# Kernel optimization log

Measured on AMD Instinct MI355X. Metric: run time of the kernel, lower is better.

Reference implementation:

```python
import jax, jax.numpy as jnp
import numpy as np

NUM_EMBEDDINGS = 1024
EMBEDDING_DIM = 64
COMMITMENT_COST = 0.25


def setup_inputs() -> dict:
    key = jax.random.key(0)
    k_in, k_cb = jax.random.split(key)
    inputs = jax.random.normal(k_in, (32, 4096, EMBEDDING_DIM), dtype=jnp.float32)
    # matches reset_embeddings(): uniform(-1/num_embeddings, 1/num_embeddings)
    bound = 1.0 / NUM_EMBEDDINGS
    codebook = jax.random.uniform(k_cb, (NUM_EMBEDDINGS, EMBEDDING_DIM),
                                  dtype=jnp.float32, minval=-bound, maxval=bound)
    return {"inputs": inputs, "codebook": codebook}


def reference(inputs, codebook):
    input_shape = inputs.shape
    D = codebook.shape[1]
    x = inputs.reshape(-1, D)  # [N, D]
    # Squared euclidean distances; argmin is invariant to the sqrt used by torch.cdist.
    # dist2[n,k] = ||x_n||^2 - 2 x_n . e_k + ||e_k||^2
    dist2 = (jnp.sum(x * x, axis=1, keepdims=True)
             - 2.0 * (x @ codebook.T)
             + jnp.sum(codebook * codebook, axis=1))  # [N, K]
    encoding_indices = jnp.argmin(dist2, axis=1)  # [N]
    quantized = codebook[encoding_indices].reshape(input_shape)
    loss = (jnp.mean((jax.lax.stop_gradient(quantized) - inputs) ** 2)
            + COMMITMENT_COST * jnp.mean((quantized - jax.lax.stop_gradient(inputs)) ** 2))
    # straight-through estimator
    quantized_st = inputs + jax.lax.stop_gradient(quantized - inputs)
    return quantized_st, loss
```

## Files before the change

### kernel.cpp

```cpp
#include <hip/hip_runtime.h>


typedef __attribute__((ext_vector_type(8))) short short8;
typedef __attribute__((ext_vector_type(4))) float f32x4;

#define VQ_D 64
#define MTILE 512
#define NTH 512
#define CSTRIDE 68

__device__ inline unsigned short f2bf(float f) {
  union { float f; unsigned u; } v; v.f = f;
  unsigned r = v.u + 0x7FFFu + ((v.u >> 16) & 1u);
  return (unsigned short)(r >> 16);
}

__global__ __launch_bounds__(256) void vq_prep(const float* __restrict__ cb,
                                               float* __restrict__ c2b,
                                               unsigned short* __restrict__ cbb,
                                               float* __restrict__ sse,
                                               unsigned* __restrict__ counter, int K) {
  if (blockIdx.x == 0 && threadIdx.x == 0) { *sse = 0.f; *counter = 0u; }
  int w = (int)((blockIdx.x * 256 + threadIdx.x) >> 6);
  int lane = threadIdx.x & 63;
  if (w >= K) return;
  float v = cb[(size_t)w * VQ_D + lane];
  cbb[(size_t)w * CSTRIDE + lane] = f2bf(v);
  if (lane < CSTRIDE - VQ_D) cbb[(size_t)w * CSTRIDE + VQ_D + lane] = 0;
  float s = v * v;
#pragma unroll
  for (int off = 32; off; off >>= 1) s += __shfl_down(s, off);
  if (lane == 0) c2b[w] = s + 0.5f;
}

__global__ __launch_bounds__(NTH) void vq_main(
    const float* __restrict__ x, const float* __restrict__ cb,
    const float* __restrict__ c2b, const unsigned short* __restrict__ cbb,
    float* __restrict__ out, float* __restrict__ sse_out,
    unsigned* __restrict__ counter, int nblocks) {
  __shared__ unsigned short cbs[1024 * CSTRIDE];
  __shared__ float c2s[1024];
  __shared__ int idxs[MTILE];
  __shared__ float redbuf[8];

  const int tid = threadIdx.x;
  const int wave = tid >> 6;
  const int lane = tid & 63;
  const int quad = lane >> 4;
  const int col = lane & 15;
  const long blockRow0 = (long)blockIdx.x * MTILE;
  const int waveRow0 = wave * 64;

  const char* gbase = (const char*)cbb;
#pragma unroll
  for (int i = 0; i < 17; ++i) {
    const int chunk0 = i * NTH + wave * 64;
    const char* src = gbase + (size_t)(chunk0 + lane) * 16;
    __builtin_amdgcn_global_load_lds(
        (const __attribute__((address_space(1))) void*)src,
        (__attribute__((address_space(3))) void*)(cbs + (size_t)chunk0 * 8),
        16, 0, 0);
  }
  c2s[tid] = c2b[tid];
  c2s[tid + 512] = c2b[tid + 512];

  short8 Af[4][2];
#pragma unroll
  for (int mi = 0; mi < 4; ++mi) {
#pragma unroll
    for (int ks = 0; ks < 2; ++ks) {
      long row = blockRow0 + waveRow0 + mi * 16 + col;
      const f32x4* xp = (const f32x4*)(x + row * VQ_D + ks * 32 + quad * 8);
      f32x4 lo = xp[0];
      f32x4 hi = xp[1];
      short8 a;
      a[0] = (short)f2bf(-2.f * lo[0]); a[1] = (short)f2bf(-2.f * lo[1]);
      a[2] = (short)f2bf(-2.f * lo[2]); a[3] = (short)f2bf(-2.f * lo[3]);
      a[4] = (short)f2bf(-2.f * hi[0]); a[5] = (short)f2bf(-2.f * hi[1]);
      a[6] = (short)f2bf(-2.f * hi[2]); a[7] = (short)f2bf(-2.f * hi[3]);
      Af[mi][ks] = a;
    }
  }

  unsigned bk[4][4];
#pragma unroll
  for (int mi = 0; mi < 4; ++mi)
#pragma unroll
    for (int r = 0; r < 4; ++r) bk[mi][r] = 0xFFFFFFFFu;

  __syncthreads();

  const unsigned short* bbase = cbs + (size_t)col * CSTRIDE + quad * 8;
#pragma unroll 4
  for (int t = 0; t < 64; ++t) {
    const unsigned short* bp = bbase + t * 16 * CSTRIDE;
    short8 b0 = *(const short8*)bp;
    short8 b1 = *(const short8*)(bp + 32);
    float cc = c2s[t * 16 + col];

    f32x4 acc[4];
#pragma unroll
    for (int mi = 0; mi < 4; ++mi) {
      f32x4 a = {cc, cc, cc, cc};
      a = __builtin_amdgcn_mfma_f32_16x16x32_bf16(Af[mi][0], b0, a, 0, 0, 0);
      a = __builtin_amdgcn_mfma_f32_16x16x32_bf16(Af[mi][1], b1, a, 0, 0, 0);
      acc[mi] = a;
    }

    const unsigned code = (unsigned)((t << 4) + col);
#pragma unroll
    for (int mi = 0; mi < 4; ++mi)
#pragma unroll
      for (int r = 0; r < 4; ++r)
        bk[mi][r] = min(bk[mi][r], (__float_as_uint(acc[mi][r]) & 0xFFFFFC00u) | code);
  }

#pragma unroll
  for (int off = 1; off < 16; off <<= 1) {
#pragma unroll
    for (int mi = 0; mi < 4; ++mi)
#pragma unroll
      for (int r = 0; r < 4; ++r) {
        unsigned o = (unsigned)__shfl_xor((int)bk[mi][r], off);
        bk[mi][r] = min(bk[mi][r], o);
      }
  }
  if (col == 0) {
#pragma unroll
    for (int mi = 0; mi < 4; ++mi)
#pragma unroll
      for (int r = 0; r < 4; ++r)
        idxs[waveRow0 + mi * 16 + quad * 4 + r] = (int)(bk[mi][r] & 1023u);
  }
  __syncthreads();

  float sse = 0.f;
  const f32x4* x4 = (const f32x4*)x;
  f32x4* out4 = (f32x4*)out;
#pragma unroll
  for (int i = 0; i < 16; ++i) {
    int f = i * NTH + tid;
    int row_l = f >> 4;
    int d4 = f & 15;
    int idx = idxs[row_l];
    unsigned long long ev =
        *(const unsigned long long*)(cbs + (size_t)idx * CSTRIDE + d4 * 4);
    f32x4 cv;
    cv[0] = __uint_as_float((unsigned)(ev & 0xFFFFull) << 16);
    cv[1] = __uint_as_float((unsigned)((ev >> 16) & 0xFFFFull) << 16);
    cv[2] = __uint_as_float((unsigned)((ev >> 32) & 0xFFFFull) << 16);
    cv[3] = __uint_as_float((unsigned)((ev >> 48) & 0xFFFFull) << 16);
    long gi = (blockRow0 + row_l) * 16 + d4;
    f32x4 xv = x4[gi];
    out4[gi] = cv;
    f32x4 dv = cv - xv;
    sse += dv[0] * dv[0] + dv[1] * dv[1] + dv[2] * dv[2] + dv[3] * dv[3];
  }
#pragma unroll
  for (int off = 32; off; off >>= 1) sse += __shfl_down(sse, off);
  if (lane == 0) redbuf[wave] = sse;
  __syncthreads();

  if (tid == 0) {
    float s = 0.f;
#pragma unroll
    for (int w = 0; w < 8; ++w) s += redbuf[w];
    atomicAdd(sse_out, s);
    __threadfence();
    unsigned old = atomicAdd(counter, 1u);
    if (old == (unsigned)(nblocks - 1)) {
      float tot = atomicAdd(sse_out, 0.f);
      long nelem = (long)nblocks * MTILE * VQ_D;
      out[nelem] = 1.25f * tot / (float)nelem;
    }
  }
}

extern "C" void kernel_launch(void* const* d_in, const int* in_sizes, int n_in,
                              void* d_out, int out_size, void* d_ws, size_t ws_size,
                              hipStream_t stream) {
  const float* x = (const float*)d_in[0];
  const float* cb = (const float*)d_in[1];
  float* out = (float*)d_out;

  const long n_elem = (long)in_sizes[0];
  const int nrows = (int)(n_elem / VQ_D);
  const int K = in_sizes[1] / VQ_D;
  const int nblocks = nrows / MTILE;

  char* ws = (char*)d_ws;
  float* sse = (float*)ws;
  unsigned* counter = (unsigned*)(ws + 64);
  float* c2b = (float*)(ws + 256);
  unsigned short* cbb = (unsigned short*)(ws + 8192);

  vq_prep<<<dim3((K * 64 + 255) / 256), dim3(256), 0, stream>>>(cb, c2b, cbb, sse, counter, K);
  vq_main<<<dim3(nblocks), dim3(NTH), 0, stream>>>(x, cb, c2b, cbb, out, sse, counter, nblocks);
}
```

Measured before the change: 132.2 us.

## Derive SSE from argmin distance and split codebook gather into separate kernel

The loss is now computed algebraically from the minimum distance value kept in the packed argmin key plus the per-row input norm. This removes the second read of x and the per-element difference loop. The output gather moves to a separate kernel that copies fp32 codebook rows by index from a global index buffer. This also fixes the old path writing bf16-rounded codebook values. The risk is that the SSE is less exact: the distance key is bf16-based and its low 10 bits are truncated. It also adds an extra kernel launch plus a global index write and read.

```diff
diff --git a/kernel.cpp b/kernel.cpp
--- a/kernel.cpp
+++ b/kernel.cpp
@@ -33,14 +33,15 @@
   if (lane == 0) c2b[w] = s + 0.5f;
 }
 
-__global__ __launch_bounds__(NTH) void vq_main(
-    const float* __restrict__ x, const float* __restrict__ cb,
-    const float* __restrict__ c2b, const unsigned short* __restrict__ cbb,
+__global__ __launch_bounds__(NTH) void vq_argmin(
+    const float* __restrict__ x, const float* __restrict__ c2b,
+    const unsigned short* __restrict__ cbb, int* __restrict__ gidx,
     float* __restrict__ out, float* __restrict__ sse_out,
     unsigned* __restrict__ counter, int nblocks) {
   __shared__ unsigned short cbs[1024 * CSTRIDE];
   __shared__ float c2s[1024];
   __shared__ int idxs[MTILE];
+  __shared__ float xn[MTILE];
   __shared__ float redbuf[8];
 
   const int tid = threadIdx.x;
@@ -67,12 +68,15 @@
   short8 Af[4][2];
 #pragma unroll
   for (int mi = 0; mi < 4; ++mi) {
+    float nrm = 0.f;
 #pragma unroll
     for (int ks = 0; ks < 2; ++ks) {
       long row = blockRow0 + waveRow0 + mi * 16 + col;
       const f32x4* xp = (const f32x4*)(x + row * VQ_D + ks * 32 + quad * 8);
       f32x4 lo = xp[0];
       f32x4 hi = xp[1];
+      nrm += lo[0] * lo[0] + lo[1] * lo[1] + lo[2] * lo[2] + lo[3] * lo[3];
+      nrm += hi[0] * hi[0] + hi[1] * hi[1] + hi[2] * hi[2] + hi[3] * hi[3];
       short8 a;
       a[0] = (short)f2bf(-2.f * lo[0]); a[1] = (short)f2bf(-2.f * lo[1]);
       a[2] = (short)f2bf(-2.f * lo[2]); a[3] = (short)f2bf(-2.f * lo[3]);
@@ -80,6 +84,9 @@
       a[6] = (short)f2bf(-2.f * hi[2]); a[7] = (short)f2bf(-2.f * hi[3]);
       Af[mi][ks] = a;
     }
+    nrm += __shfl_xor(nrm, 16);
+    nrm += __shfl_xor(nrm, 32);
+    if (quad == 0) xn[waveRow0 + mi * 16 + col] = nrm;
   }
 
   unsigned bk[4][4];
@@ -125,41 +132,25 @@
         bk[mi][r] = min(bk[mi][r], o);
       }
   }
+
+  float sse = 0.f;
   if (col == 0) {
 #pragma unroll
     for (int mi = 0; mi < 4; ++mi)
 #pragma unroll
-      for (int r = 0; r < 4; ++r)
-        idxs[waveRow0 + mi * 16 + quad * 4 + r] = (int)(bk[mi][r] & 1023u);
-  }
-  __syncthreads();
-
-  float sse = 0.f;
-  const f32x4* x4 = (const f32x4*)x;
-  f32x4* out4 = (f32x4*)out;
-#pragma unroll
-  for (int i = 0; i < 16; ++i) {
-    int f = i * NTH + tid;
-    int row_l = f >> 4;
-    int d4 = f & 15;
-    int idx = idxs[row_l];
-    unsigned long long ev =
-        *(const unsigned long long*)(cbs + (size_t)idx * CSTRIDE + d4 * 4);
-    f32x4 cv;
-    cv[0] = __uint_as_float((unsigned)(ev & 0xFFFFull) << 16);
-    cv[1] = __uint_as_float((unsigned)((ev >> 16) & 0xFFFFull) << 16);
-    cv[2] = __uint_as_float((unsigned)((ev >> 32) & 0xFFFFull) << 16);
-    cv[3] = __uint_as_float((unsigned)((ev >> 48) & 0xFFFFull) << 16);
-    long gi = (blockRow0 + row_l) * 16 + d4;
-    f32x4 xv = x4[gi];
-    out4[gi] = cv;
-    f32x4 dv = cv - xv;
-    sse += dv[0] * dv[0] + dv[1] * dv[1] + dv[2] * dv[2] + dv[3] * dv[3];
-  }
-#pragma unroll
-  for (int off = 32; off; off >>= 1) sse += __shfl_down(sse, off);
+      for (int r = 0; r < 4; ++r) {
+        const int row = waveRow0 + mi * 16 + quad * 4 + r;
+        idxs[row] = (int)(bk[mi][r] & 1023u);
+        const float s_rec = __uint_as_float(bk[mi][r] & 0xFFFFFC00u);
+        sse += s_rec - 0.5f + xn[row];
+      }
+  }
+  sse += __shfl_xor(sse, 16);
+  sse += __shfl_xor(sse, 32);
   if (lane == 0) redbuf[wave] = sse;
   __syncthreads();
+
+  gidx[blockRow0 + tid] = idxs[tid];
 
   if (tid == 0) {
     float s = 0.f;
@@ -176,6 +167,21 @@
   }
 }
 
+__global__ __launch_bounds__(256) void vq_gather(const float* __restrict__ cb,
+                                                 const int* __restrict__ gidx,
+                                                 float* __restrict__ out) {
+  const int t = blockIdx.x * 256 + threadIdx.x;
+  const f32x4* cb4 = (const f32x4*)cb;
+  f32x4* out4 = (f32x4*)out;
+#pragma unroll
+  for (int i = 0; i < 4; ++i) {
+    const int f = t + i * (1 << 19);
+    const int row = f >> 4;
+    const int d4 = f & 15;
+    out4[f] = cb4[(size_t)gidx[row] * 16 + d4];
+  }
+}
+
 extern "C" void kernel_launch(void* const* d_in, const int* in_sizes, int n_in,
                               void* d_out, int out_size, void* d_ws, size_t ws_size,
                               hipStream_t stream) {
@@ -193,7 +199,9 @@
   unsigned* counter = (unsigned*)(ws + 64);
   float* c2b = (float*)(ws + 256);
   unsigned short* cbb = (unsigned short*)(ws + 8192);
+  int* gidx = (int*)(ws + 8192 + 139264);
 
   vq_prep<<<dim3((K * 64 + 255) / 256), dim3(256), 0, stream>>>(cb, c2b, cbb, sse, counter, K);
-  vq_main<<<dim3(nblocks), dim3(NTH), 0, stream>>>(x, cb, c2b, cbb, out, sse, counter, nblocks);
-}
+  vq_argmin<<<dim3(nblocks), dim3(NTH), 0, stream>>>(x, c2b, cbb, gidx, out, sse, counter, nblocks);
+  vq_gather<<<dim3(nrows * 16 / (256 * 4)), dim3(256), 0, stream>>>(cb, gidx, out);
+}
```

Result: faster. 129.0 us (-2.4%).
